# Kernel optimization log

Hardware: AMD Instinct MI355X
Metric: run time of the kernel (lower is better)

## Reference

```python
import jax, jax.numpy as jnp
import numpy as np

B, N, GEO, CLS = 32, 1024, 4, 28
F0 = GEO + CLS          # 32
F1 = F0 * 2             # 64
F2 = F0 * 4             # 128
EPS = 1e-5


def _lin(x, W, b):
    return x @ W.T + b


def _bn(x, g, b):
    # torch BatchNorm1d(element_num) on [B, N, F]: channel dim is N,
    # normalize over (batch, feature) with biased variance (training mode).
    m = x.mean(axis=(0, 2), keepdims=True)
    v = ((x - m) ** 2).mean(axis=(0, 2), keepdims=True)
    return g[None, :, None] * (x - m) * jax.lax.rsqrt(v + EPS) + b[None, :, None]


def _relation(x, Wu, bu, psi, phi, wr):
    # Vectorized form of the triple python loop:
    #   S[b,i,j] = psi*phi * <x_i, x_j>, diagonal excluded
    #   out_i   = wr * (sum_j S[b,i,j] * relu(unary(x_j))) / N + x_i
    n = x.shape[1]
    U = jax.nn.relu(_lin(x, Wu, bu))                       # [B,N,F2]
    S = (psi[0] * phi[0]) * jnp.einsum('bnd,bmd->bnm', x, x)
    S = S * (1.0 - jnp.eye(n, dtype=x.dtype))              # mask i==j
    return wr[0] * (S @ U) / n + x


def setup_inputs() -> dict:
    key = jax.random.key(0)
    ks = iter(jax.random.split(key, 64))

    def W(o, i):
        return jax.random.normal(next(ks), (o, i), jnp.float32) * 0.02

    def bvec(o):
        return jnp.zeros((o,), jnp.float32)

    inp = {'input': jax.random.uniform(next(ks), (B, N, F0), jnp.float32)}
    inp.update(e1_W=W(F1, F0), e1_b=bvec(F1),
               bn1_g=jnp.ones((N,), jnp.float32), bn1_b=bvec(N),
               e2_W=W(F2, F1), e2_b=bvec(F2),
               bn2_g=jnp.ones((N,), jnp.float32), bn2_b=bvec(N),
               e3_W=W(F2, F2), e3_b=bvec(F2))
    for r in (1, 2, 3, 4):
        inp[f'r{r}_W'] = W(F2, F2)
        inp[f'r{r}_b'] = bvec(F2)
        inp[f'r{r}_psi'] = jax.random.uniform(next(ks), (1,), jnp.float32)
        inp[f'r{r}_phi'] = jax.random.uniform(next(ks), (1,), jnp.float32)
        inp[f'r{r}_wr'] = jax.random.uniform(next(ks), (1,), jnp.float32)
    inp.update(d1_W=W(F1, F2), d1_b=bvec(F1),
               dbn_g=jnp.ones((N,), jnp.float32), dbn_b=bvec(N),
               d2_W=W(F0, F1), d2_b=bvec(F0),
               bc_W=W(CLS, F0), bc_b=bvec(CLS),
               bg_W=W(GEO, F0), bg_b=bvec(GEO))
    return inp


def reference(input, e1_W, e1_b, bn1_g, bn1_b, e2_W, e2_b, bn2_g, bn2_b,
              e3_W, e3_b,
              r1_W, r1_b, r1_psi, r1_phi, r1_wr,
              r2_W, r2_b, r2_psi, r2_phi, r2_wr,
              r3_W, r3_b, r3_psi, r3_phi, r3_wr,
              r4_W, r4_b, r4_psi, r4_phi, r4_wr,
              d1_W, d1_b, dbn_g, dbn_b, d2_W, d2_b,
              bc_W, bc_b, bg_W, bg_b):
    out = jax.nn.relu(_bn(_lin(input, e1_W, e1_b), bn1_g, bn1_b))
    out = jax.nn.relu(_bn(_lin(out, e2_W, e2_b), bn2_g, bn2_b))
    enc = jax.nn.sigmoid(_lin(out, e3_W, e3_b))
    x = _relation(enc, r1_W, r1_b, r1_psi, r1_phi, r1_wr)
    x = _relation(x, r2_W, r2_b, r2_psi, r2_phi, r2_wr)
    x = _relation(x, r3_W, r3_b, r3_psi, r3_phi, r3_wr)
    x = _relation(x, r4_W, r4_b, r4_psi, r4_phi, r4_wr)
    out = jax.nn.relu(_bn(_lin(x, d1_W, d1_b), dbn_g, dbn_b))
    out = jax.nn.relu(_lin(out, d2_W, d2_b))
    syn_cls = _lin(out, bc_W, bc_b)
    syn_geo = _lin(out, bg_W, bg_b)
    return jnp.concatenate((syn_cls, syn_geo), axis=2)
```

## Files before the change

kernel.cpp:

```cpp
#include <hip/hip_runtime.h>
#include <hip/hip_bf16.h>


typedef __hip_bfloat16 bf16;
typedef unsigned short ushort_t;
typedef float v4f __attribute__((ext_vector_type(4)));
typedef short v8s __attribute__((ext_vector_type(8)));
#define MFMA_BF16 __builtin_amdgcn_mfma_f32_16x16x32_bf16

#define NB 32
#define NN 1024
#define XSTRIDE 72

__device__ __forceinline__ float ldin(const void* p, size_t i, int f32){
    return f32 ? ((const float*)p)[i] : __bfloat162float(((const bf16*)p)[i]);
}
__device__ __forceinline__ float bf2f(ushort_t u){
    return __uint_as_float((unsigned)u << 16);
}
__device__ __forceinline__ ushort_t f2bf(float v){
    bf16 h = __float2bfloat16(v);
    ushort_t s; __builtin_memcpy(&s, &h, 2);
    return s;
}
__device__ __forceinline__ void unpack8(uint4 v, float* f){
    f[0] = __uint_as_float(v.x << 16);
    f[1] = __uint_as_float(v.x & 0xffff0000u);
    f[2] = __uint_as_float(v.y << 16);
    f[3] = __uint_as_float(v.y & 0xffff0000u);
    f[4] = __uint_as_float(v.z << 16);
    f[5] = __uint_as_float(v.z & 0xffff0000u);
    f[6] = __uint_as_float(v.w << 16);
    f[7] = __uint_as_float(v.w & 0xffff0000u);
}

__device__ __forceinline__ int detect_dev(const void* inp){
    __shared__ int sflag;
    int t = threadIdx.x;
    if (t < 64){
        unsigned v = ((const unsigned*)inp)[t];
        unsigned long long m = __ballot((v & 0x80008000u) != 0u);
        if (t == 0) sflag = (__popcll(m) > 4) ? 1 : 0;
    }
    __syncthreads();
    return sflag;
}

struct PrepArgs {
    const void* w[11];
    int K[11], O[11], off[11];
};

__global__ __launch_bounds__(256) void k_prep(PrepArgs a, float* __restrict__ wpf,
                                              ushort_t* __restrict__ whi, ushort_t* __restrict__ wlo,
                                              const void* __restrict__ detin){
    int f32 = detect_dev(detin);
    int s = blockIdx.y;
    int idx = blockIdx.x*256 + threadIdx.x;
    if (s < 6){
        int K = a.K[s], O = a.O[s];
        if (idx >= K*O) return;
        int k = idx / O, j = idx - k*O;
        wpf[a.off[s] + idx] = ldin(a.w[s], (size_t)j*K + k, f32);
    } else {
        if (idx >= 16384) return;
        int n = idx >> 7, k = idx & 127;
        float v = ldin(a.w[s], (size_t)n*128 + k, f32);
        ushort_t h = f2bf(v);
        ushort_t l = f2bf(v - bf2f(h));
        int di = (s - 6)*16384 + ((k >> 3)*128 + n)*8 + (k & 7);
        whi[di] = h; wlo[di] = l;
    }
}

__global__ __launch_bounds__(128) void k_bnlin12(
    const void* __restrict__ xin,
    const float* __restrict__ Wt1, const void* __restrict__ b1v,
    const void* __restrict__ g1, const void* __restrict__ bb1,
    const float* __restrict__ Wt2, const void* __restrict__ b2v,
    const void* __restrict__ g2, const void* __restrict__ bb2,
    ushort_t* __restrict__ out, const void* __restrict__ detin)
{
    int f32 = detect_dev(detin);
    __shared__ __align__(16) float wt1[32*64];
    __shared__ __align__(16) float wt2[64*128];
    __shared__ __align__(16) float xst[2][32*36];
    __shared__ __align__(16) float cst[2][64*36];
    int t = threadIdx.x;
    int w = t >> 6, lane = t & 63;
    int n = blockIdx.x*2 + w;

    for (int i = t; i < 32*64/4; i += 128)
        ((float4*)wt1)[i] = ((const float4*)Wt1)[i];
    for (int i = t; i < 64*128/4; i += 128)
        ((float4*)wt2)[i] = ((const float4*)Wt2)[i];
    for (int i = lane; i < 32*4; i += 64){
        int b = i >> 2, g = i & 3;
        float f[8];
        if (f32){
            const float* src = (const float*)xin + ((size_t)b*NN + n)*32 + g*8;
            float4 v0 = ((const float4*)src)[0];
            float4 v1 = ((const float4*)src)[1];
            f[0]=v0.x; f[1]=v0.y; f[2]=v0.z; f[3]=v0.w;
            f[4]=v1.x; f[5]=v1.y; f[6]=v1.z; f[7]=v1.w;
        } else {
            uint4 v = *(const uint4*)((const ushort_t*)xin + ((size_t)b*NN + n)*32 + (size_t)g*8);
            unpack8(v, f);
        }
        #pragma unroll
        for (int j=0;j<8;j++) xst[w][(g*8+j)*36 + b] = f[j];
    }
    __syncthreads();

    {
        int b0 = (lane & 7)*4, j0 = (lane >> 3)*8;
        float acc[4][8];
        #pragma unroll
        for (int i=0;i<4;i++)
            #pragma unroll
            for (int j=0;j<8;j++) acc[i][j] = 0.f;
        for (int k = 0; k < 32; k++){
            float xv[4], wv[8];
            *(float4*)&xv[0] = *(const float4*)&xst[w][k*36 + b0];
            *(float4*)&wv[0] = *(const float4*)&wt1[k*64 + j0];
            *(float4*)&wv[4] = *(const float4*)&wt1[k*64 + j0 + 4];
            #pragma unroll
            for (int i=0;i<4;i++)
                #pragma unroll
                for (int j=0;j<8;j++) acc[i][j] = fmaf(xv[i], wv[j], acc[i][j]);
        }
        float bj[8];
        #pragma unroll
        for (int j=0;j<8;j++) bj[j] = ldin(b1v, j0+j, f32);
        float s1 = 0.f, s2 = 0.f;
        #pragma unroll
        for (int i=0;i<4;i++)
            #pragma unroll
            for (int j=0;j<8;j++){
                float a = acc[i][j] + bj[j];
                acc[i][j] = a; s1 += a; s2 = fmaf(a, a, s2);
            }
        #pragma unroll
        for (int off = 32; off > 0; off >>= 1){
            s1 += __shfl_down(s1, off);
            s2 += __shfl_down(s2, off);
        }
        s1 = __shfl(s1, 0); s2 = __shfl(s2, 0);
        float m  = s1 / 2048.f;
        float vv = s2 / 2048.f - m*m;
        float rs = rsqrtf(vv + 1e-5f);
        float gv = ldin(g1, n, f32), bv = ldin(bb1, n, f32);
        #pragma unroll
        for (int i=0;i<4;i++)
            #pragma unroll
            for (int j=0;j<8;j++)
                cst[w][(j0+j)*36 + b0+i] =
                    fmaxf(fmaf(gv*(acc[i][j]-m), rs, bv), 0.f);
    }
    __syncthreads();

    {
        int b0 = (lane & 3)*8, j0 = (lane >> 2)*8;
        float acc[8][8];
        #pragma unroll
        for (int i=0;i<8;i++)
            #pragma unroll
            for (int j=0;j<8;j++) acc[i][j] = 0.f;
        for (int k = 0; k < 64; k++){
            float xv[8], wv[8];
            *(float4*)&xv[0] = *(const float4*)&cst[w][k*36 + b0];
            *(float4*)&xv[4] = *(const float4*)&cst[w][k*36 + b0 + 4];
            *(float4*)&wv[0] = *(const float4*)&wt2[k*128 + j0];
            *(float4*)&wv[4] = *(const float4*)&wt2[k*128 + j0 + 4];
            #pragma unroll
            for (int i=0;i<8;i++)
                #pragma unroll
                for (int j=0;j<8;j++) acc[i][j] = fmaf(xv[i], wv[j], acc[i][j]);
        }
        float bj[8];
        #pragma unroll
        for (int j=0;j<8;j++) bj[j] = ldin(b2v, j0+j, f32);
        float s1 = 0.f, s2 = 0.f;
        #pragma unroll
        for (int i=0;i<8;i++)
            #pragma unroll
            for (int j=0;j<8;j++){
                float a = acc[i][j] + bj[j];
                acc[i][j] = a; s1 += a; s2 = fmaf(a, a, s2);
            }
        #pragma unroll
        for (int off = 32; off > 0; off >>= 1){
            s1 += __shfl_down(s1, off);
            s2 += __shfl_down(s2, off);
        }
        s1 = __shfl(s1, 0); s2 = __shfl(s2, 0);
        float m  = s1 / 4096.f;
        float vv = s2 / 4096.f - m*m;
        float rs = rsqrtf(vv + 1e-5f);
        float gv = ldin(g2, n, f32), bv = ldin(bb2, n, f32);
        #pragma unroll
        for (int i=0;i<8;i++){
            union { uint4 u; ushort_t s[8]; } pk;
            #pragma unroll
            for (int j=0;j<8;j++)
                pk.s[j] = f2bf(fmaxf(fmaf(gv*(acc[i][j]-m), rs, bv), 0.f));
            *(uint4*)(out + ((size_t)(b0+i)*NN + n)*128 + j0) = pk.u;
        }
    }
}

template<int K, int O>
__global__ __launch_bounds__(128) void k_bnlin(
    const ushort_t* __restrict__ xin, const float* __restrict__ Wt,
    const void* __restrict__ bias, const void* __restrict__ bng,
    const void* __restrict__ bnb, ushort_t* __restrict__ out,
    const void* __restrict__ detin)
{
    int f32 = detect_dev(detin);
    constexpr int BR  = O/16;
    constexpr int NBT = 32/BR;
    constexpr int G   = K/8;
    __shared__ __align__(16) float wt[K*O];
    __shared__ __align__(16) float xst[2][K*36];
    int t = threadIdx.x;
    int w = t >> 6, lane = t & 63;
    int n = blockIdx.x*2 + w;

    for (int i = t; i < K*O/4; i += 128)
        ((float4*)wt)[i] = ((const float4*)Wt)[i];
    for (int i = lane; i < 32*G; i += 64){
        int b = i / G, g = i - b*G;
        float f[8];
        uint4 v = *(const uint4*)(xin + ((size_t)b*NN + n)*K + (size_t)g*8);
        unpack8(v, f);
        #pragma unroll
        for (int j=0;j<8;j++) xst[w][(g*8+j)*36 + b] = f[j];
    }
    __syncthreads();

    int bt = lane % NBT, jt = lane / NBT;
    int b0 = bt*BR, j0 = jt*8;
    const float* xw = xst[w];
    float acc[BR][8];
    #pragma unroll
    for (int i=0;i<BR;i++)
        #pragma unroll
        for (int j=0;j<8;j++) acc[i][j] = 0.f;

    for (int k = 0; k < K; k++){
        float xv[BR], wv[8];
        #pragma unroll
        for (int i=0;i<BR;i+=4)
            *(float4*)&xv[i] = *(const float4*)&xw[k*36 + b0 + i];
        *(float4*)&wv[0] = *(const float4*)&wt[k*O + j0];
        *(float4*)&wv[4] = *(const float4*)&wt[k*O + j0 + 4];
        #pragma unroll
        for (int i=0;i<BR;i++)
            #pragma unroll
            for (int j=0;j<8;j++) acc[i][j] = fmaf(xv[i], wv[j], acc[i][j]);
    }

    float bj[8];
    #pragma unroll
    for (int j=0;j<8;j++) bj[j] = ldin(bias, j0+j, f32);
    float s1 = 0.f, s2 = 0.f;
    #pragma unroll
    for (int i=0;i<BR;i++)
        #pragma unroll
        for (int j=0;j<8;j++){
            float a = acc[i][j] + bj[j];
            acc[i][j] = a; s1 += a; s2 = fmaf(a, a, s2);
        }
    #pragma unroll
    for (int off = 32; off > 0; off >>= 1){
        s1 += __shfl_down(s1, off);
        s2 += __shfl_down(s2, off);
    }
    s1 = __shfl(s1, 0); s2 = __shfl(s2, 0);
    const float M = 32.f * O;
    float m  = s1 / M;
    float vv = s2 / M - m*m;
    float rs = rsqrtf(vv + 1e-5f);
    float gv = ldin(bng, n, f32), bv = ldin(bnb, n, f32);
    #pragma unroll
    for (int i=0;i<BR;i++){
        union { uint4 u; ushort_t s[8]; } pk;
        #pragma unroll
        for (int j=0;j<8;j++)
            pk.s[j] = f2bf(fmaxf(fmaf(gv*(acc[i][j]-m), rs, bv), 0.f));
        *(uint4*)(out + ((size_t)(b0+i)*NN + n)*O + j0) = pk.u;
    }
}


__device__ __forceinline__ void tail_stage_x(ushort_t* xs, ushort_t* xt,
                                             const float o[2][16],
                                             int w, int col, int quad){
    #pragma unroll
    for (int nt=0;nt<2;nt++){
        int n = w*32 + nt*16 + col;
        #pragma unroll
        for (int m=0;m<4;m++){
            union { uint2 u2; ushort_t s[4]; } pk;
            #pragma unroll
            for (int reg=0;reg<4;reg++){
                int r = m*16 + quad*4 + reg;
                ushort_t hv = f2bf(o[nt][m*4+reg]);
                xs[((n>>3)*64 + r)*8 + (n&7)] = hv;
                pk.s[reg] = hv;
            }
            *(uint2*)&xt[n*XSTRIDE + m*16 + quad*4] = pk.u2;
        }
    }
}

__device__ __forceinline__ void tail_write_A(const ushort_t* xs, ushort_t* A,
                                             size_t row0, int t){
    uint4* dst = (uint4*)(A + row0*128);
    #pragma unroll
    for (int c = 0; c < 4; c++){
        int i = t + c*256;
        int r = i >> 4, kg = i & 15;
        dst[i] = *(const uint4*)&xs[(kg*64 + r)*8];
    }
}

__device__ __forceinline__ void mfma_hilo(const ushort_t* xs,
    const ushort_t* Bh, const ushort_t* Bl, v4f acc[4][2],
    int w, int col, int quad)
{
    #pragma unroll
    for (int m=0;m<4;m++)
        #pragma unroll
        for (int nt=0;nt<2;nt++) acc[m][nt] = (v4f){0.f,0.f,0.f,0.f};
    #pragma unroll
    for (int kt = 0; kt < 4; kt++){
        int kg = kt*4 + quad;
        v8s a[4], bh[2], bl[2];
        #pragma unroll
        for (int nt=0;nt<2;nt++){
            int n = w*32 + nt*16 + col;
            bh[nt] = *(const v8s*)&Bh[(kg*128 + n)*8];
            bl[nt] = *(const v8s*)&Bl[(kg*128 + n)*8];
        }
        #pragma unroll
        for (int m=0;m<4;m++)
            a[m] = *(const v8s*)&xs[(kg*64 + m*16 + col)*8];
        #pragma unroll
        for (int m=0;m<4;m++)
            #pragma unroll
            for (int nt=0;nt<2;nt++){
                acc[m][nt] = MFMA_BF16(a[m], bh[nt], acc[m][nt], 0, 0, 0);
                acc[m][nt] = MFMA_BF16(a[m], bl[nt], acc[m][nt], 0, 0, 0);
            }
    }
}

__device__ __forceinline__ void tail_lin_relu_T(ushort_t* xs, ushort_t* xt,
    const ushort_t* Whi, const ushort_t* Wlo, const void* bias,
    ushort_t* Tp, size_t row0, int t, int w, int col, int quad, int f32)
{
    v4f acc[4][2];
    mfma_hilo(xs, Whi, Wlo, acc, w, col, quad);
    float u[2][16];
    #pragma unroll
    for (int nt=0;nt<2;nt++){
        int n = w*32 + nt*16 + col;
        float bn = ldin(bias, n, f32);
        #pragma unroll
        for (int m=0;m<4;m++)
            #pragma unroll
            for (int reg=0;reg<4;reg++)
                u[nt][m*4+reg] = fmaxf(acc[m][nt][reg] + bn, 0.f);
    }
    __syncthreads();
    #pragma unroll
    for (int nt=0;nt<2;nt++){
        int n = w*32 + nt*16 + col;
        #pragma unroll
        for (int m=0;m<4;m++){
            union { uint2 u2; ushort_t s[4]; } pk;
            #pragma unroll
            for (int reg=0;reg<4;reg++)
                pk.s[reg] = f2bf(u[nt][m*4+reg]);
            *(uint2*)&xs[n*XSTRIDE + m*16 + quad*4] = pk.u2;
        }
    }
    __syncthreads();
    v4f tacc[4][4];
    #pragma unroll
    for (int m=0;m<4;m++)
        #pragma unroll
        for (int q=0;q<4;q++) tacc[m][q] = (v4f){0.f,0.f,0.f,0.f};
    int wn = (w & 1)*64, wc = (w >> 1)*64;
    #pragma unroll
    for (int kt = 0; kt < 2; kt++){
        int kg = kt*4 + quad;
        v8s a[4], bb[4];
        #pragma unroll
        for (int m=0;m<4;m++)
            a[m] = *(const v8s*)&xs[(wn + m*16 + col)*XSTRIDE + kg*8];
        #pragma unroll
        for (int q=0;q<4;q++)
            bb[q] = *(const v8s*)&xt[(wc + q*16 + col)*XSTRIDE + kg*8];
        #pragma unroll
        for (int m=0;m<4;m++)
            #pragma unroll
            for (int q=0;q<4;q++)
                tacc[m][q] = MFMA_BF16(a[m], bb[q], tacc[m][q], 0, 0, 0);
    }
    int s16 = (int)((row0 >> 6) & 15);
    int b   = (int)(row0 >> 10);
    ushort_t* dst = Tp + ((size_t)(s16*NB + b) << 14);
    #pragma unroll
    for (int m=0;m<4;m++)
        #pragma unroll
        for (int q=0;q<4;q++){
            int c = wc + q*16 + col;
            union { uint2 u2; ushort_t s[4]; } pk;
            #pragma unroll
            for (int reg=0;reg<4;reg++)
                pk.s[reg] = f2bf(tacc[m][q][reg]);
            *(uint2*)&dst[c*128 + wn + m*16 + quad*4] = pk.u2;
        }
}

__global__ __launch_bounds__(256) void k_linfuse0(
    const ushort_t* __restrict__ xin,
    const ushort_t* __restrict__ W3h, const ushort_t* __restrict__ W3l,
    const void* __restrict__ b3,
    const ushort_t* __restrict__ W1h, const ushort_t* __restrict__ W1l,
    const void* __restrict__ b1,
    ushort_t* __restrict__ A, ushort_t* __restrict__ Tp,
    const void* __restrict__ detin)
{
    __shared__ __align__(16) ushort_t xs[128*XSTRIDE];
    __shared__ __align__(16) ushort_t xt[128*XSTRIDE];
    int f32 = detect_dev(detin);
    int t = threadIdx.x;
    size_t row0 = (size_t)blockIdx.x * 64;
    {
        const uint4* src = (const uint4*)(xin + row0*128);
        #pragma unroll
        for (int c = 0; c < 4; c++){
            int i = t + c*256;
            int r = i >> 4, kg = i & 15;
            *(uint4*)&xs[(kg*64 + r)*8] = src[i];
        }
    }
    __syncthreads();
    int w = t >> 6, lane = t & 63;
    int col = lane & 15, quad = lane >> 4;
    v4f acc[4][2];
    mfma_hilo(xs, W3h, W3l, acc, w, col, quad);
    float o[2][16];
    #pragma unroll
    for (int nt=0;nt<2;nt++){
        int n = w*32 + nt*16 + col;
        float bn = ldin(b3, n, f32);
        #pragma unroll
        for (int m=0;m<4;m++)
            #pragma unroll
            for (int reg=0;reg<4;reg++){
                float v = acc[m][nt][reg] + bn;
                o[nt][m*4+reg] = 1.f/(1.f+expf(-v));
            }
    }
    __syncthreads();
    tail_stage_x(xs, xt, o, w, col, quad);
    __syncthreads();
    tail_write_A(xs, A, row0, t);
    tail_lin_relu_T(xs, xt, W1h, W1l, b1, Tp, row0, t, w, col, quad, f32);
}

__global__ __launch_bounds__(256) void k_tredb(const ushort_t* __restrict__ Tp,
                                               ushort_t* __restrict__ Thi, ushort_t* __restrict__ Tlo){
    int tau = blockIdx.x*256 + threadIdx.x;
    int b = tau >> 11;
    int j2 = tau & 2047;
    int cg = j2 >> 7, n = j2 & 127;
    float sum[8] = {0,0,0,0,0,0,0,0};
    #pragma unroll
    for (int s = 0; s < 16; s++){
        const ushort_t* src = Tp + ((size_t)(s*NB + b) << 14) + cg*8*128 + n;
        #pragma unroll
        for (int cc = 0; cc < 8; cc++)
            sum[cc] += bf2f(src[cc*128]);
    }
    union { uint4 u; ushort_t s[8]; } ph, pl;
    #pragma unroll
    for (int cc = 0; cc < 8; cc++){
        ushort_t h = f2bf(sum[cc]);
        ph.s[cc] = h;
        pl.s[cc] = f2bf(sum[cc] - bf2f(h));
    }
    size_t di = ((size_t)b << 14) + ((size_t)cg*128 + n)*8;
    *(uint4*)&Thi[di] = ph.u;
    *(uint4*)&Tlo[di] = pl.u;
}

template<int LAST>
__global__ __launch_bounds__(256) void k_relfuse(
    ushort_t* __restrict__ x,
    const ushort_t* __restrict__ Thi, const ushort_t* __restrict__ Tlo,
    const void* __restrict__ psi, const void* __restrict__ phi, const void* __restrict__ wr,
    const ushort_t* __restrict__ Wrh, const ushort_t* __restrict__ Wrl,
    const void* __restrict__ rbias,
    const ushort_t* __restrict__ Wnh, const ushort_t* __restrict__ Wnl,
    const void* __restrict__ bnext, ushort_t* __restrict__ Tp,
    const void* __restrict__ detin)
{
    __shared__ __align__(16) ushort_t xs[128*XSTRIDE];
    __shared__ __align__(16) ushort_t xt[128*XSTRIDE];
    __shared__ __align__(16) float sdvec[64];
    int f32 = detect_dev(detin);
    int t = threadIdx.x;
    size_t row0 = (size_t)blockIdx.x * 64;
    int b = (int)(row0 >> 10);
    {
        const uint4* src = (const uint4*)(x + row0*128);
        #pragma unroll
        for (int c = 0; c < 4; c++){
            int i = t + c*256;
            int r = i >> 4, kg = i & 15;
            *(uint4*)&xs[(kg*64 + r)*8] = src[i];
        }
    }
    __syncthreads();
    int w = t >> 6, lane = t & 63;
    int col = lane & 15, quad = lane >> 4;

    if (t < 64){
        float s = 0.f;
        #pragma unroll 8
        for (int k=0;k<128;k++){
            float v = bf2f(xs[((k>>3)*64 + t)*8 + (k&7)]);
            s = fmaf(v, v, s);
        }
        sdvec[t] = s;
    }
    {
        v4f uacc[4][2];
        mfma_hilo(xs, Wrh, Wrl, uacc, w, col, quad);
        #pragma unroll
        for (int nt=0;nt<2;nt++){
            int n = w*32 + nt*16 + col;
            float bn = ldin(rbias, n, f32);
            #pragma unroll
            for (int m=0;m<4;m++){
                union { uint2 u2; ushort_t s[4]; } pk;
                #pragma unroll
                for (int reg=0;reg<4;reg++)
                    pk.s[reg] = f2bf(fmaxf(uacc[m][nt][reg] + bn, 0.f));
                *(uint2*)&xt[n*XSTRIDE + m*16 + quad*4] = pk.u2;
            }
        }
    }
    __syncthreads();

    float alpha = ldin(wr,0,f32) * ldin(psi,0,f32) * ldin(phi,0,f32) * (1.f/1024.f);
    const ushort_t* sh = Thi + ((size_t)b << 14);
    const ushort_t* sl = Tlo + ((size_t)b << 14);
    v4f acc[4][2];
    mfma_hilo(xs, sh, sl, acc, w, col, quad);
    float o[2][16];
    #pragma unroll
    for (int m=0;m<4;m++){
        float4 d4 = *(const float4*)&sdvec[m*16 + quad*4];
        const float* dr = (const float*)&d4;
        #pragma unroll
        for (int nt=0;nt<2;nt++){
            int n = w*32 + nt*16 + col;
            #pragma unroll
            for (int reg=0;reg<4;reg++){
                int r = m*16 + quad*4 + reg;
                float ufv = bf2f(xt[n*XSTRIDE + r]);
                float xv = bf2f(xs[((n>>3)*64 + r)*8 + (n&7)]);
                o[nt][m*4+reg] = fmaf(alpha, acc[m][nt][reg] - dr[reg]*ufv, xv);
            }
        }
    }
    __syncthreads();
    tail_stage_x(xs, xt, o, w, col, quad);
    __syncthreads();
    tail_write_A(xs, x, row0, t);
    if (!LAST)
        tail_lin_relu_T(xs, xt, Wnh, Wnl, bnext, Tp,
                        row0, t, w, col, quad, f32);
}

__global__ __launch_bounds__(256) void k_dec2(
    const ushort_t* __restrict__ x,
    const float* __restrict__ W2t, const void* __restrict__ b2,
    const float* __restrict__ Wct, const void* __restrict__ bcb,
    const float* __restrict__ Wgt, const void* __restrict__ bgb,
    void* __restrict__ out, const void* __restrict__ detin)
{
    int f32 = detect_dev(detin);
    __shared__ __align__(16) float w2[64*32];
    __shared__ __align__(16) float wc[32*28];
    __shared__ __align__(16) float wg[32*4];
    __shared__ __align__(16) float xsd[8][64];
    __shared__ float hs[8][33];
    int t = threadIdx.x;
    for (int i=t;i<512;i+=256)  ((float4*)w2)[i] = ((const float4*)W2t)[i];
    if (t < 224) ((float4*)wc)[t] = ((const float4*)Wct)[t];
    if (t < 32)  ((float4*)wg)[t] = ((const float4*)Wgt)[t];
    int j = t & 31, r = t >> 5;
    for (int tile = blockIdx.x; tile < 4096; tile += 512){
        size_t row0 = (size_t)tile * 8;
        __syncthreads();
        if (t < 64){
            int row = t >> 3, seg = t & 7;
            uint4 v = *(const uint4*)&x[(row0 + row)*64 + seg*8];
            float f[8]; unpack8(v, f);
            *(float4*)&xsd[row][seg*8]   = make_float4(f[0],f[1],f[2],f[3]);
            *(float4*)&xsd[row][seg*8+4] = make_float4(f[4],f[5],f[6],f[7]);
        }
        __syncthreads();
        float a = ldin(b2, j, f32);
        #pragma unroll 8
        for (int k=0;k<64;k++) a = fmaf(xsd[r][k], w2[k*32 + j], a);
        hs[r][j] = fmaxf(a, 0.f);
        __syncthreads();
        float o;
        if (j < 28){
            o = ldin(bcb, j, f32);
            #pragma unroll
            for (int k=0;k<32;k++) o = fmaf(hs[r][k], wc[k*28 + j], o);
        } else {
            int jj = j - 28;
            o = ldin(bgb, jj, f32);
            #pragma unroll
            for (int k=0;k<32;k++) o = fmaf(hs[r][k], wg[k*4 + jj], o);
        }
        size_t oi = (row0 + r)*32 + j;
        if (f32) ((float*)out)[oi] = o;
        else     ((ushort_t*)out)[oi] = f2bf(o);
    }
}

enum { O_E1=0, O_E2=2048, O_D1=10240, O_D2=18432, O_BC=20480, O_BG=21376 };

extern "C" void kernel_launch(void* const* d_in, const int* in_sizes, int n_in,
                              void* d_out, int out_size, void* d_ws, size_t ws_size,
                              hipStream_t stream)
{
    (void)in_sizes; (void)n_in; (void)out_size; (void)ws_size;
    const void* input = d_in[0];
    const void* e1_W = d_in[1];  const void* e1_b = d_in[2];
    const void* bn1_g = d_in[3]; const void* bn1_b = d_in[4];
    const void* e2_W = d_in[5];  const void* e2_b = d_in[6];
    const void* bn2_g = d_in[7]; const void* bn2_b = d_in[8];
    const void* e3_W = d_in[9];  const void* e3_b = d_in[10];
    const void *rW[4], *rb[4], *rpsi[4], *rphi[4], *rwr[4];
    for (int r = 0; r < 4; r++){
        rW[r]   = d_in[11 + r*5 + 0];
        rb[r]   = d_in[11 + r*5 + 1];
        rpsi[r] = d_in[11 + r*5 + 2];
        rphi[r] = d_in[11 + r*5 + 3];
        rwr[r]  = d_in[11 + r*5 + 4];
    }
    const void* d1_W = d_in[31]; const void* d1_b = d_in[32];
    const void* dbn_g = d_in[33];const void* dbn_b = d_in[34];
    const void* d2_W = d_in[35]; const void* d2_b = d_in[36];
    const void* bc_W = d_in[37]; const void* bc_b = d_in[38];
    const void* bg_W = d_in[39]; const void* bg_b = d_in[40];

    float*    ws_f = (float*)d_ws;
    float*    wpf  = ws_f;
    ushort_t* whi  = (ushort_t*)(ws_f + 54272);
    ushort_t* wlo  = (ushort_t*)(ws_f + 95232);
    ushort_t* Thi  = (ushort_t*)(ws_f + 136192);
    ushort_t* Tlo  = (ushort_t*)(ws_f + 398336);
    ushort_t* Tp   = (ushort_t*)(ws_f + 660480);
    ushort_t* A    = (ushort_t*)(ws_f + 4854784);
    ushort_t* Cdec = (ushort_t*)(ws_f + 6951936);
    ushort_t* E2   = (ushort_t*)(ws_f + 9049088);

    PrepArgs pa;
    const void* srcs[11] = {e1_W, e2_W, d1_W, d2_W, bc_W, bg_W,
                            e3_W, rW[0], rW[1], rW[2], rW[3]};
    const int  Ks[11]   = {32,64,128,64,32,32, 128,128,128,128,128};
    const int  Os[11]   = {64,128,64,32,28,4,  128,128,128,128,128};
    const int  offs[11] = {O_E1,O_E2,O_D1,O_D2,O_BC,O_BG, 0,0,0,0,0};
    for (int i=0;i<11;i++){ pa.w[i]=srcs[i]; pa.K[i]=Ks[i]; pa.O[i]=Os[i]; pa.off[i]=offs[i]; }

    k_prep<<<dim3(64,11), 256, 0, stream>>>(pa, wpf, whi, wlo, input);
    k_bnlin12<<<512, 128, 0, stream>>>(input,
                                       wpf+O_E1, e1_b, bn1_g, bn1_b,
                                       wpf+O_E2, e2_b, bn2_g, bn2_b,
                                       E2, input);
    k_linfuse0<<<512, 256, 0, stream>>>(E2, whi, wlo, e3_b,
                                        whi + 16384, wlo + 16384, rb[0],
                                        A, Tp, input);

    for (int r = 0; r < 4; r++){
        k_tredb<<<256, 256, 0, stream>>>(Tp, Thi, Tlo);
        if (r < 3)
            k_relfuse<0><<<512, 256, 0, stream>>>(A, Thi, Tlo,
                rpsi[r], rphi[r], rwr[r],
                whi + (size_t)(1+r)*16384, wlo + (size_t)(1+r)*16384, rb[r],
                whi + (size_t)(2+r)*16384, wlo + (size_t)(2+r)*16384, rb[r+1],
                Tp, input);
        else
            k_relfuse<1><<<512, 256, 0, stream>>>(A, Thi, Tlo,
                rpsi[r], rphi[r], rwr[r],
                whi + (size_t)4*16384, wlo + (size_t)4*16384, rb[3],
                whi, wlo, rb[0],
                Tp, input);
    }

    k_bnlin<128,64><<<512, 128, 0, stream>>>(A, wpf+O_D1, d1_b, dbn_g, dbn_b, Cdec, input);
    k_dec2<<<512, 256, 0, stream>>>(Cdec, wpf+O_D2, d2_b, wpf+O_BC, bc_b, wpf+O_BG, bg_b, d_out, input);
}
```

Measured before the change: 300.4 us.

## Fuse weight prep into encoder kernel and decoder stages into one tail kernel

The separate weight-prep kernel is folded into the encoder kernel as extra blocks, and the encoder now loads and transposes e1/e2 weights itself from raw inputs. The decoder BN-linear and the final small linears are merged into one kernel that keeps the intermediate activations in shared memory, removing the Cdec round-trip through global memory and two launches. The trade is larger shared-memory use per block and extra strided, uncoalesced weight loads repeated in every encoder block.

```diff
diff --git a/kernel.cpp b/kernel.cpp
--- a/kernel.cpp
+++ b/kernel.cpp
@@ -47,53 +47,54 @@
 }
 
 struct PrepArgs {
-    const void* w[11];
-    int K[11], O[11], off[11];
+    const void* w[9];
+    int K[9], O[9], off[9];
 };
 
-__global__ __launch_bounds__(256) void k_prep(PrepArgs a, float* __restrict__ wpf,
-                                              ushort_t* __restrict__ whi, ushort_t* __restrict__ wlo,
-                                              const void* __restrict__ detin){
-    int f32 = detect_dev(detin);
-    int s = blockIdx.y;
-    int idx = blockIdx.x*256 + threadIdx.x;
-    if (s < 6){
-        int K = a.K[s], O = a.O[s];
-        if (idx >= K*O) return;
-        int k = idx / O, j = idx - k*O;
-        wpf[a.off[s] + idx] = ldin(a.w[s], (size_t)j*K + k, f32);
-    } else {
-        if (idx >= 16384) return;
-        int n = idx >> 7, k = idx & 127;
-        float v = ldin(a.w[s], (size_t)n*128 + k, f32);
-        ushort_t h = f2bf(v);
-        ushort_t l = f2bf(v - bf2f(h));
-        int di = (s - 6)*16384 + ((k >> 3)*128 + n)*8 + (k & 7);
-        whi[di] = h; wlo[di] = l;
-    }
-}
-
-__global__ __launch_bounds__(128) void k_bnlin12(
+__global__ __launch_bounds__(128) void k_enc0(PrepArgs a, float* __restrict__ wpf,
+    ushort_t* __restrict__ whi, ushort_t* __restrict__ wlo,
     const void* __restrict__ xin,
-    const float* __restrict__ Wt1, const void* __restrict__ b1v,
+    const void* __restrict__ e1w, const void* __restrict__ b1v,
     const void* __restrict__ g1, const void* __restrict__ bb1,
-    const float* __restrict__ Wt2, const void* __restrict__ b2v,
+    const void* __restrict__ e2w, const void* __restrict__ b2v,
     const void* __restrict__ g2, const void* __restrict__ bb2,
     ushort_t* __restrict__ out, const void* __restrict__ detin)
 {
     int f32 = detect_dev(detin);
+    int t = threadIdx.x;
+
+    if (blockIdx.x >= 512){
+        int p = blockIdx.x - 512;
+        int s = p >> 7;
+        int idx = (p & 127)*128 + t;
+        if (s < 4){
+            int K = a.K[s], O = a.O[s];
+            if (idx >= K*O) return;
+            int k = idx / O, j = idx - k*O;
+            wpf[a.off[s] + idx] = ldin(a.w[s], (size_t)j*K + k, f32);
+        } else {
+            if (idx >= 16384) return;
+            int n = idx >> 7, k = idx & 127;
+            float v = ldin(a.w[s], (size_t)n*128 + k, f32);
+            ushort_t h = f2bf(v);
+            ushort_t l = f2bf(v - bf2f(h));
+            int di = (s - 4)*16384 + ((k >> 3)*128 + n)*8 + (k & 7);
+            whi[di] = h; wlo[di] = l;
+        }
+        return;
+    }
+
     __shared__ __align__(16) float wt1[32*64];
     __shared__ __align__(16) float wt2[64*128];
     __shared__ __align__(16) float xst[2][32*36];
     __shared__ __align__(16) float cst[2][64*36];
-    int t = threadIdx.x;
     int w = t >> 6, lane = t & 63;
     int n = blockIdx.x*2 + w;
 
-    for (int i = t; i < 32*64/4; i += 128)
-        ((float4*)wt1)[i] = ((const float4*)Wt1)[i];
-    for (int i = t; i < 64*128/4; i += 128)
-        ((float4*)wt2)[i] = ((const float4*)Wt2)[i];
+    for (int i = t; i < 2048; i += 128)
+        wt1[(i & 31)*64 + (i >> 5)] = ldin(e1w, i, f32);
+    for (int i = t; i < 8192; i += 128)
+        wt2[(i & 63)*128 + (i >> 6)] = ldin(e2w, i, f32);
     for (int i = lane; i < 32*4; i += 64){
         int b = i >> 2, g = i & 3;
         float f[8];
@@ -137,8 +138,8 @@
         for (int i=0;i<4;i++)
             #pragma unroll
             for (int j=0;j<8;j++){
-                float a = acc[i][j] + bj[j];
-                acc[i][j] = a; s1 += a; s2 = fmaf(a, a, s2);
+                float a2 = acc[i][j] + bj[j];
+                acc[i][j] = a2; s1 += a2; s2 = fmaf(a2, a2, s2);
             }
         #pragma unroll
         for (int off = 32; off > 0; off >>= 1){
@@ -185,8 +186,8 @@
         for (int i=0;i<8;i++)
             #pragma unroll
             for (int j=0;j<8;j++){
-                float a = acc[i][j] + bj[j];
-                acc[i][j] = a; s1 += a; s2 = fmaf(a, a, s2);
+                float a2 = acc[i][j] + bj[j];
+                acc[i][j] = a2; s1 += a2; s2 = fmaf(a2, a2, s2);
             }
         #pragma unroll
         for (int off = 32; off > 0; off >>= 1){
@@ -209,67 +210,64 @@
     }
 }
 
-template<int K, int O>
-__global__ __launch_bounds__(128) void k_bnlin(
-    const ushort_t* __restrict__ xin, const float* __restrict__ Wt,
-    const void* __restrict__ bias, const void* __restrict__ bng,
-    const void* __restrict__ bnb, ushort_t* __restrict__ out,
-    const void* __restrict__ detin)
+__global__ __launch_bounds__(128) void k_dectail(
+    const ushort_t* __restrict__ xin,
+    const float* __restrict__ W1t,
+    const void* __restrict__ d1b, const void* __restrict__ bng,
+    const void* __restrict__ bnb,
+    const float* __restrict__ W2t,
+    const void* __restrict__ b2,
+    const float* __restrict__ Wct, const void* __restrict__ bcb,
+    const float* __restrict__ Wgt, const void* __restrict__ bgb,
+    void* __restrict__ out, const void* __restrict__ detin)
 {
+    __shared__ __align__(16) float smem[8192 + 9216];
+    float* wt  = smem;
+    float* xst = smem + 8192;
     int f32 = detect_dev(detin);
-    constexpr int BR  = O/16;
-    constexpr int NBT = 32/BR;
-    constexpr int G   = K/8;
-    __shared__ __align__(16) float wt[K*O];
-    __shared__ __align__(16) float xst[2][K*36];
     int t = threadIdx.x;
     int w = t >> 6, lane = t & 63;
     int n = blockIdx.x*2 + w;
 
-    for (int i = t; i < K*O/4; i += 128)
-        ((float4*)wt)[i] = ((const float4*)Wt)[i];
-    for (int i = lane; i < 32*G; i += 64){
-        int b = i / G, g = i - b*G;
+    for (int i = t; i < 8192/4; i += 128)
+        ((float4*)wt)[i] = ((const float4*)W1t)[i];
+    float* xw = xst + w*4608;
+    for (int i = lane; i < 32*16; i += 64){
+        int b = i >> 4, g = i & 15;
         float f[8];
-        uint4 v = *(const uint4*)(xin + ((size_t)b*NN + n)*K + (size_t)g*8);
+        uint4 v = *(const uint4*)(xin + ((size_t)b*NN + n)*128 + (size_t)g*8);
         unpack8(v, f);
         #pragma unroll
-        for (int j=0;j<8;j++) xst[w][(g*8+j)*36 + b] = f[j];
-    }
-    __syncthreads();
-
-    int bt = lane % NBT, jt = lane / NBT;
-    int b0 = bt*BR, j0 = jt*8;
-    const float* xw = xst[w];
-    float acc[BR][8];
-    #pragma unroll
-    for (int i=0;i<BR;i++)
+        for (int j=0;j<8;j++) xw[(g*8+j)*36 + b] = f[j];
+    }
+    __syncthreads();
+
+    int b0 = (lane & 7)*4, j0 = (lane >> 3)*8;
+    float acc[4][8];
+    #pragma unroll
+    for (int i=0;i<4;i++)
         #pragma unroll
         for (int j=0;j<8;j++) acc[i][j] = 0.f;
-
-    for (int k = 0; k < K; k++){
-        float xv[BR], wv[8];
-        #pragma unroll
-        for (int i=0;i<BR;i+=4)
-            *(float4*)&xv[i] = *(const float4*)&xw[k*36 + b0 + i];
-        *(float4*)&wv[0] = *(const float4*)&wt[k*O + j0];
-        *(float4*)&wv[4] = *(const float4*)&wt[k*O + j0 + 4];
-        #pragma unroll
-        for (int i=0;i<BR;i++)
+    for (int k = 0; k < 128; k++){
+        float xv[4], wv[8];
+        *(float4*)&xv[0] = *(const float4*)&xw[k*36 + b0];
+        *(float4*)&wv[0] = *(const float4*)&wt[k*64 + j0];
+        *(float4*)&wv[4] = *(const float4*)&wt[k*64 + j0 + 4];
+        #pragma unroll
+        for (int i=0;i<4;i++)
             #pragma unroll
             for (int j=0;j<8;j++) acc[i][j] = fmaf(xv[i], wv[j], acc[i][j]);
     }
-
     float bj[8];
     #pragma unroll
-    for (int j=0;j<8;j++) bj[j] = ldin(bias, j0+j, f32);
+    for (int j=0;j<8;j++) bj[j] = ldin(d1b, j0+j, f32);
     float s1 = 0.f, s2 = 0.f;
     #pragma unroll
-    for (int i=0;i<BR;i++)
+    for (int i=0;i<4;i++)
         #pragma unroll
         for (int j=0;j<8;j++){
-            float a = acc[i][j] + bj[j];
-            acc[i][j] = a; s1 += a; s2 = fmaf(a, a, s2);
+            float a2 = acc[i][j] + bj[j];
+            acc[i][j] = a2; s1 += a2; s2 = fmaf(a2, a2, s2);
         }
     #pragma unroll
     for (int off = 32; off > 0; off >>= 1){
@@ -277,21 +275,61 @@
         s2 += __shfl_down(s2, off);
     }
     s1 = __shfl(s1, 0); s2 = __shfl(s2, 0);
-    const float M = 32.f * O;
-    float m  = s1 / M;
-    float vv = s2 / M - m*m;
+    float m  = s1 / 2048.f;
+    float vv = s2 / 2048.f - m*m;
     float rs = rsqrtf(vv + 1e-5f);
     float gv = ldin(bng, n, f32), bv = ldin(bnb, n, f32);
-    #pragma unroll
-    for (int i=0;i<BR;i++){
-        union { uint4 u; ushort_t s[8]; } pk;
-        #pragma unroll
-        for (int j=0;j<8;j++)
-            pk.s[j] = f2bf(fmaxf(fmaf(gv*(acc[i][j]-m), rs, bv), 0.f));
-        *(uint4*)(out + ((size_t)(b0+i)*NN + n)*O + j0) = pk.u;
-    }
-}
-
+    __syncthreads();
+
+    float* w2s  = wt;
+    float* wcs  = wt + 2048;
+    float* wgs  = wt + 2944;
+    float* cstw = xst + w*2080;
+    float* hsw  = xst + 4160 + w*1056;
+    for (int i = t; i < 512; i += 128) ((float4*)w2s)[i] = ((const float4*)W2t)[i];
+    for (int i = t; i < 224; i += 128) ((float4*)wcs)[i] = ((const float4*)Wct)[i];
+    if (t < 32) ((float4*)wgs)[t] = ((const float4*)Wgt)[t];
+    #pragma unroll
+    for (int i=0;i<4;i++)
+        #pragma unroll
+        for (int j=0;j<8;j++){
+            float val = fmaxf(fmaf(gv*(acc[i][j]-m), rs, bv), 0.f);
+            cstw[(b0+i)*65 + (j0+j)] = bf2f(f2bf(val));
+        }
+    __syncthreads();
+
+    int b = lane & 31, jg = lane >> 5;
+    float h[16];
+    #pragma unroll
+    for (int jj=0;jj<16;jj++) h[jj] = ldin(b2, jg*16+jj, f32);
+    for (int k = 0; k < 64; k++){
+        float xv = cstw[b*65 + k];
+        #pragma unroll
+        for (int jj=0;jj<16;jj++)
+            h[jj] = fmaf(xv, w2s[k*32 + jg*16 + jj], h[jj]);
+    }
+    #pragma unroll
+    for (int jj=0;jj<16;jj++) hsw[b*33 + jg*16 + jj] = fmaxf(h[jj], 0.f);
+    __syncthreads();
+    #pragma unroll
+    for (int jj=0;jj<16;jj++){
+        int j2 = jg*16 + jj;
+        float o;
+        if (j2 < 28){
+            o = ldin(bcb, j2, f32);
+            #pragma unroll
+            for (int k=0;k<32;k++) o = fmaf(hsw[b*33 + k], wcs[k*28 + j2], o);
+        } else {
+            int gg = j2 - 28;
+            o = ldin(bgb, gg, f32);
+            #pragma unroll
+            for (int k=0;k<32;k++) o = fmaf(hsw[b*33 + k], wgs[k*4 + gg], o);
+        }
+        size_t oi = ((size_t)b*NN + n)*32 + j2;
+        if (f32) ((float*)out)[oi] = o;
+        else     ((ushort_t*)out)[oi] = f2bf(o);
+    }
+}
 
 __device__ __forceinline__ void tail_stage_x(ushort_t* xs, ushort_t* xt,
                                              const float o[2][16],
@@ -589,57 +627,6 @@
                         row0, t, w, col, quad, f32);
 }
 
-__global__ __launch_bounds__(256) void k_dec2(
-    const ushort_t* __restrict__ x,
-    const float* __restrict__ W2t, const void* __restrict__ b2,
-    const float* __restrict__ Wct, const void* __restrict__ bcb,
-    const float* __restrict__ Wgt, const void* __restrict__ bgb,
-    void* __restrict__ out, const void* __restrict__ detin)
-{
-    int f32 = detect_dev(detin);
-    __shared__ __align__(16) float w2[64*32];
-    __shared__ __align__(16) float wc[32*28];
-    __shared__ __align__(16) float wg[32*4];
-    __shared__ __align__(16) float xsd[8][64];
-    __shared__ float hs[8][33];
-    int t = threadIdx.x;
-    for (int i=t;i<512;i+=256)  ((float4*)w2)[i] = ((const float4*)W2t)[i];
-    if (t < 224) ((float4*)wc)[t] = ((const float4*)Wct)[t];
-    if (t < 32)  ((float4*)wg)[t] = ((const float4*)Wgt)[t];
-    int j = t & 31, r = t >> 5;
-    for (int tile = blockIdx.x; tile < 4096; tile += 512){
-        size_t row0 = (size_t)tile * 8;
-        __syncthreads();
-        if (t < 64){
-            int row = t >> 3, seg = t & 7;
-            uint4 v = *(const uint4*)&x[(row0 + row)*64 + seg*8];
-            float f[8]; unpack8(v, f);
-            *(float4*)&xsd[row][seg*8]   = make_float4(f[0],f[1],f[2],f[3]);
-            *(float4*)&xsd[row][seg*8+4] = make_float4(f[4],f[5],f[6],f[7]);
-        }
-        __syncthreads();
-        float a = ldin(b2, j, f32);
-        #pragma unroll 8
-        for (int k=0;k<64;k++) a = fmaf(xsd[r][k], w2[k*32 + j], a);
-        hs[r][j] = fmaxf(a, 0.f);
-        __syncthreads();
-        float o;
-        if (j < 28){
-            o = ldin(bcb, j, f32);
-            #pragma unroll
-            for (int k=0;k<32;k++) o = fmaf(hs[r][k], wc[k*28 + j], o);
-        } else {
-            int jj = j - 28;
-            o = ldin(bgb, jj, f32);
-            #pragma unroll
-            for (int k=0;k<32;k++) o = fmaf(hs[r][k], wg[k*4 + jj], o);
-        }
-        size_t oi = (row0 + r)*32 + j;
-        if (f32) ((float*)out)[oi] = o;
-        else     ((ushort_t*)out)[oi] = f2bf(o);
-    }
-}
-
 enum { O_E1=0, O_E2=2048, O_D1=10240, O_D2=18432, O_BC=20480, O_BG=21376 };
 
 extern "C" void kernel_launch(void* const* d_in, const int* in_sizes, int n_in,
@@ -675,22 +662,20 @@
     ushort_t* Tlo  = (ushort_t*)(ws_f + 398336);
     ushort_t* Tp   = (ushort_t*)(ws_f + 660480);
     ushort_t* A    = (ushort_t*)(ws_f + 4854784);
-    ushort_t* Cdec = (ushort_t*)(ws_f + 6951936);
     ushort_t* E2   = (ushort_t*)(ws_f + 9049088);
 
     PrepArgs pa;
-    const void* srcs[11] = {e1_W, e2_W, d1_W, d2_W, bc_W, bg_W,
-                            e3_W, rW[0], rW[1], rW[2], rW[3]};
-    const int  Ks[11]   = {32,64,128,64,32,32, 128,128,128,128,128};
-    const int  Os[11]   = {64,128,64,32,28,4,  128,128,128,128,128};
-    const int  offs[11] = {O_E1,O_E2,O_D1,O_D2,O_BC,O_BG, 0,0,0,0,0};
-    for (int i=0;i<11;i++){ pa.w[i]=srcs[i]; pa.K[i]=Ks[i]; pa.O[i]=Os[i]; pa.off[i]=offs[i]; }
-
-    k_prep<<<dim3(64,11), 256, 0, stream>>>(pa, wpf, whi, wlo, input);
-    k_bnlin12<<<512, 128, 0, stream>>>(input,
-                                       wpf+O_E1, e1_b, bn1_g, bn1_b,
-                                       wpf+O_E2, e2_b, bn2_g, bn2_b,
-                                       E2, input);
+    const void* srcs[9] = {d1_W, d2_W, bc_W, bg_W,
+                           e3_W, rW[0], rW[1], rW[2], rW[3]};
+    const int  Ks[9]   = {128,64,32,32, 128,128,128,128,128};
+    const int  Os[9]   = {64,32,28,4,   128,128,128,128,128};
+    const int  offs[9] = {O_D1,O_D2,O_BC,O_BG, 0,0,0,0,0};
+    for (int i=0;i<9;i++){ pa.w[i]=srcs[i]; pa.K[i]=Ks[i]; pa.O[i]=Os[i]; pa.off[i]=offs[i]; }
+
+    k_enc0<<<512 + 9*128, 128, 0, stream>>>(pa, wpf, whi, wlo,
+                                            input, e1_W, e1_b, bn1_g, bn1_b,
+                                            e2_W, e2_b, bn2_g, bn2_b,
+                                            E2, input);
     k_linfuse0<<<512, 256, 0, stream>>>(E2, whi, wlo, e3_b,
                                         whi + 16384, wlo + 16384, rb[0],
                                         A, Tp, input);
@@ -711,6 +696,7 @@
                 Tp, input);
     }
 
-    k_bnlin<128,64><<<512, 128, 0, stream>>>(A, wpf+O_D1, d1_b, dbn_g, dbn_b, Cdec, input);
-    k_dec2<<<512, 256, 0, stream>>>(Cdec, wpf+O_D2, d2_b, wpf+O_BC, bc_b, wpf+O_BG, bg_b, d_out, input);
-}
+    k_dectail<<<512, 128, 0, stream>>>(A, wpf+O_D1, d1_b, dbn_g, dbn_b,
+                                       wpf+O_D2, d2_b, wpf+O_BC, bc_b,
+                                       wpf+O_BG, bg_b, d_out, input);
+}
```

Measured after the change: 311.1 us. +3.6%, slower.
